# Kernel tuning notes

Measured on AMD Instinct MI355X. Metric: run time of the kernel, lower is better.

The kernel has to match this reference:

```python
import jax, jax.numpy as jnp
import numpy as np

B, H, W, C = 32, 56, 56, 256
NH, WS, SH = 8, 7, 3
HD = C // NH
SCALE = HD ** -0.5
N = WS * WS
MLP = 4 * C


def _rel_pos_index():
    coords = np.stack(np.meshgrid(np.arange(WS), np.arange(WS), indexing='ij')).reshape(2, -1)
    rel = (coords[:, :, None] - coords[:, None, :]).transpose(1, 2, 0)
    rel[..., 0] += WS - 1
    rel[..., 1] += WS - 1
    rel[..., 0] *= 2 * WS - 1
    return jnp.asarray(rel.sum(-1))  # (N, N) int


def _attn_mask():
    # standard Swin shifted-window mask, computed statically
    img = np.zeros((H, W))
    cnt = 0
    for hs in (slice(0, -WS), slice(-WS, -SH), slice(-SH, None)):
        for ws_ in (slice(0, -WS), slice(-WS, -SH), slice(-SH, None)):
            img[hs, ws_] = cnt
            cnt += 1
    mw = img.reshape(H // WS, WS, W // WS, WS).transpose(0, 2, 1, 3).reshape(-1, N)
    am = mw[:, None, :] - mw[:, :, None]
    am = np.where(am != 0, -1e9, 0.0).astype(np.float32)
    return jnp.asarray(am)  # (nW, N, N)


def _part(x):
    b = x.shape[0]
    x = x.reshape(b, H // WS, WS, W // WS, WS, C)
    return x.transpose(0, 1, 3, 2, 4, 5).reshape(-1, N, C)


def _rev(xw):
    x = xw.reshape(-1, H // WS, W // WS, WS, WS, C)
    return x.transpose(0, 1, 3, 2, 4, 5).reshape(-1, H, W, C)


def _ln(x, g, b):
    m = x.mean(-1, keepdims=True)
    v = x.var(-1, keepdims=True)
    return (x - m) / jnp.sqrt(v + 1e-5) * g + b


def setup_inputs() -> dict:
    key = jax.random.key(0)
    ks = jax.random.split(key, 6)
    s = 0.02
    return {
        'x': jax.random.normal(ks[0], (B, H, W, C), jnp.float32),
        'gamma1': jnp.ones((C,), jnp.float32),
        'beta1': jnp.zeros((C,), jnp.float32),
        'w_qkv': jax.random.normal(ks[1], (C, 3 * C), jnp.float32) * s,
        'b_qkv': jnp.zeros((3 * C,), jnp.float32),
        'rpb': jax.random.normal(ks[2], ((2 * WS - 1) ** 2, NH), jnp.float32) * s,
        'w_proj': jax.random.normal(ks[3], (C, C), jnp.float32) * s,
        'b_proj': jnp.zeros((C,), jnp.float32),
        'gamma2': jnp.ones((C,), jnp.float32),
        'beta2': jnp.zeros((C,), jnp.float32),
        'w_fc1': jax.random.normal(ks[4], (C, MLP), jnp.float32) * s,
        'b_fc1': jnp.zeros((MLP,), jnp.float32),
        'w_fc2': jax.random.normal(ks[5], (MLP, C), jnp.float32) * s,
        'b_fc2': jnp.zeros((C,), jnp.float32),
    }


def reference(x, gamma1, beta1, w_qkv, b_qkv, rpb, w_proj, b_proj, gamma2, beta2, w_fc1, b_fc1, w_fc2, b_fc2):
    idx = _rel_pos_index()
    mask = _attn_mask()  # (nW, N, N)
    nW = mask.shape[0]

    shortcut = x
    xn = _ln(x, gamma1, beta1)
    xs = jnp.roll(xn, (-SH, -SH), axis=(1, 2))        # cyclic shift
    xw = _part(xs)                                     # (B*nW, N, C)

    qkv = (xw @ w_qkv + b_qkv).reshape(-1, N, 3, NH, HD).transpose(2, 0, 3, 1, 4)
    # SNN-variant IF (ReLU) gates on q, k, v
    q, k, v = jax.nn.relu(qkv[0]), jax.nn.relu(qkv[1]), jax.nn.relu(qkv[2])

    attn = jnp.einsum('bhnd,bhmd->bhnm', q * SCALE, k)  # (B*nW, NH, N, N)
    bias = rpb[idx].transpose(2, 0, 1)                  # (NH, N, N)
    attn = attn + bias[None]
    attn = attn.reshape(-1, nW, NH, N, N) + mask[None, :, None]
    attn = attn.reshape(-1, NH, N, N)
    # stdp_qk ReLU before softmax (faithful to source)
    attn = jax.nn.softmax(jax.nn.relu(attn), axis=-1)
    # stdp_av ReLU on attention output
    out = jax.nn.relu(jnp.einsum('bhnm,bhmd->bhnd', attn, v))
    out = out.transpose(0, 2, 1, 3).reshape(-1, N, C) @ w_proj + b_proj

    xs = _rev(out)
    x = shortcut + jnp.roll(xs, (SH, SH), axis=(1, 2))  # reverse shift + residual

    h = jax.nn.gelu(_ln(x, gamma2, beta2) @ w_fc1 + b_fc1, approximate=False)
    return x + h @ w_fc2 + b_fc2
```

## Files before the change

kernel.cpp:

```cpp
#include <hip/hip_runtime.h>
#include <stdint.h>

typedef unsigned short u16;
typedef short bf16x8 __attribute__((ext_vector_type(8)));
typedef float f32x4 __attribute__((ext_vector_type(4)));

#define NTOK 100352
#define NWIN 2048
#define CC 256
#define NHEAD 8
#define HDIM 32
#define NWT 49
#define MLPD 1024
#define ATT_SCALE 0.17677669529663687f

__device__ __forceinline__ u16 f2b(float f) {
  union { float f; uint32_t u; } c; c.f = f;
  return (u16)((c.u + 0x7fffu + ((c.u >> 16) & 1u)) >> 16);
}
__device__ __forceinline__ float b2f(u16 h) {
  union { uint32_t u; float f; } c; c.u = ((uint32_t)h) << 16;
  return c.f;
}
__device__ __forceinline__ uint32_t f2b2(float lo, float hi) {
  uint32_t r;
  asm("v_cvt_pk_bf16_f32 %0, %1, %2" : "=v"(r) : "v"(lo), "v"(hi));
  return r;
}

__device__ __forceinline__ void gload_lds16(const void* g, void* l) {
  __builtin_amdgcn_global_load_lds((const __attribute__((address_space(1))) void*)g,
                                   (__attribute__((address_space(3))) void*)l, 16, 0, 0);
}

__global__ __launch_bounds__(256)
void prep_k(const float* __restrict__ wqkv, const float* __restrict__ wproj,
            const float* __restrict__ wfc1, const float* __restrict__ wfc2,
            const float* __restrict__ rpb,
            u16* __restrict__ qkvT, u16* __restrict__ projT,
            u16* __restrict__ fc1T, u16* __restrict__ fc2T, float* __restrict__ lut) {
  int i = blockIdx.x * 256 + threadIdx.x;
  if (i < 196608) {
    int k = i / 768, n = i % 768;
    qkvT[(size_t)n * 256 + k] = f2b(wqkv[i]);
  } else if (i < 262144) {
    int j = i - 196608, k = j / 256, n = j % 256;
    projT[(size_t)n * 256 + k] = f2b(wproj[j]);
  } else if (i < 524288) {
    int j = i - 262144, k = j / 1024, n = j % 1024;
    fc1T[(size_t)n * 256 + k] = f2b(wfc1[j]);
  } else if (i < 786432) {
    int j = i - 524288, k = j / 256, n = j % 256;
    fc2T[(size_t)n * 1024 + k] = f2b(wfc2[j]);
  } else if (i < 819200) {
    int j = i - 786432;
    int h = j >> 12, m = (j >> 6) & 63, n = j & 63;
    float v = 0.f;
    if (m < 49 && n < 49) {
      int i1 = n / 7, j1 = n % 7, i2 = m / 7, j2 = m % 7;
      v = rpb[((i1 - i2 + 6) * 13 + (j1 - j2 + 6)) * 8 + h];
    }
    lut[j] = v;
  }
}

__global__ __launch_bounds__(256)
void ln_k(const float* __restrict__ x, const float* __restrict__ g,
          const float* __restrict__ be, u16* __restrict__ out) {
  int token = blockIdx.x * 4 + (threadIdx.x >> 6);
  int lane = threadIdx.x & 63;
  int win = token / 49, nn = token % 49;
  int b = win >> 6, wh = (win >> 3) & 7, ww = win & 7;
  int i = nn / 7, j = nn % 7;
  int h = wh * 7 + i + 3; if (h >= 56) h -= 56;
  int w = ww * 7 + j + 3; if (w >= 56) w -= 56;
  size_t src = ((size_t)((b * 56 + h) * 56 + w)) * CC;
  f32x4 v = *(const f32x4*)&x[src + lane * 4];
  float s1 = v[0] + v[1] + v[2] + v[3];
  float s2 = v[0]*v[0] + v[1]*v[1] + v[2]*v[2] + v[3]*v[3];
#pragma unroll
  for (int o = 32; o; o >>= 1) { s1 += __shfl_xor(s1, o); s2 += __shfl_xor(s2, o); }
  float mean = s1 * (1.f / 256.f);
  float var = s2 * (1.f / 256.f) - mean * mean;
  float rstd = rsqrtf(var + 1e-5f);
  f32x4 gv = *(const f32x4*)&g[lane * 4];
  f32x4 bv = *(const f32x4*)&be[lane * 4];
  float y0 = (v[0]-mean)*rstd*gv[0] + bv[0];
  float y1 = (v[1]-mean)*rstd*gv[1] + bv[1];
  float y2 = (v[2]-mean)*rstd*gv[2] + bv[2];
  float y3 = (v[3]-mean)*rstd*gv[3] + bv[3];
  *(uint2*)&out[(size_t)token * CC + lane * 4] = make_uint2(f2b2(y0, y1), f2b2(y2, y3));
}

#define BM 128
#define BN 128
enum { EPI_QKV = 0, EPI_GELU = 2, EPI_FC2 = 3 };

template<int EPI, int NKT>
__global__ __launch_bounds__(256)
void gemm_k(const u16* __restrict__ A, const u16* __restrict__ BT,
            const float* __restrict__ bias,
            void* __restrict__ p0, const void* __restrict__ p1) {
  constexpr int K = NKT * 64;
  __shared__ u16 aL[2][BM * 64];
  __shared__ u16 bL[BN * 64];
  const int tid = threadIdx.x;
  const int lane = tid & 63;
  const int wv = tid >> 6;
  const int wm = wv >> 1, wn = wv & 1;

  int bx = blockIdx.x, by = blockIdx.y;
  {
    int nwg = gridDim.x * gridDim.y;
    int lin = by * gridDim.x + bx;
    int q = nwg >> 3, r = nwg & 7;
    int xcd = lin & 7, idx = lin >> 3;
    int wg = (xcd < r ? xcd * (q + 1) : r * (q + 1) + (xcd - r) * q) + idx;
    bx = wg % gridDim.x;
    by = wg / gridDim.x;
  }
  const long m0 = (long)by * BM;
  const int n0 = bx * BN;

  f32x4 acc[4][4] = {};
  const int r15 = lane & 15;
  const int g4 = lane >> 4;

  const u16* pA[4];
  const u16* pB[4];
  int lslot[4];
#pragma unroll
  for (int it = 0; it < 4; ++it) {
    int slot = tid + 256 * it;
    int row = slot >> 3, c8 = slot & 7;
    int cs = c8 ^ (row & 7);
    pA[it] = &A[(m0 + row) * K + cs * 8];
    pB[it] = &BT[(size_t)(n0 + row) * K + cs * 8];
    lslot[it] = slot * 8;
  }
  int aoff[2][4], boff[2][4];
#pragma unroll
  for (int kk = 0; kk < 2; ++kk)
#pragma unroll
    for (int m = 0; m < 4; ++m) {
      int rowa = wm * 64 + m * 16 + r15;
      aoff[kk][m] = rowa * 64 + (((kk * 4 + g4) ^ (rowa & 7)) << 3);
      int rowb = wn * 64 + m * 16 + r15;
      boff[kk][m] = rowb * 64 + (((kk * 4 + g4) ^ (rowb & 7)) << 3);
    }

  auto stageA = [&](int bufi) {
#pragma unroll
    for (int it = 0; it < 4; ++it) { gload_lds16(pA[it], &aL[bufi][lslot[it]]); pA[it] += 64; }
  };
  auto stageB = [&]() {
#pragma unroll
    for (int it = 0; it < 4; ++it) { gload_lds16(pB[it], &bL[lslot[it]]); pB[it] += 64; }
  };

  stageB();
  stageA(0);
  stageA(1);

  for (int t = 0; t < NKT; ++t) {
    if (t + 1 < NKT) asm volatile("s_waitcnt vmcnt(4)" ::: "memory");
    else             asm volatile("s_waitcnt vmcnt(0)" ::: "memory");
    __builtin_amdgcn_sched_barrier(0);
    __builtin_amdgcn_s_barrier();
    __builtin_amdgcn_sched_barrier(0);
    {
      const u16* ab = aL[t & 1];
#pragma unroll
      for (int kk = 0; kk < 2; ++kk) {
        bf16x8 af[4], bfr[4];
#pragma unroll
        for (int m = 0; m < 4; ++m) af[m] = *(const bf16x8*)&ab[aoff[kk][m]];
#pragma unroll
        for (int n = 0; n < 4; ++n) bfr[n] = *(const bf16x8*)&bL[boff[kk][n]];
#pragma unroll
        for (int n = 0; n < 4; ++n)
#pragma unroll
          for (int m = 0; m < 4; ++m)
            acc[n][m] = __builtin_amdgcn_mfma_f32_16x16x32_bf16(bfr[n], af[m], acc[n][m], 0, 0, 0);
      }
    }
    __builtin_amdgcn_sched_barrier(0);
    __builtin_amdgcn_s_barrier();
    __builtin_amdgcn_sched_barrier(0);
    if (t + 1 < NKT) stageB();
    if (t + 2 < NKT) stageA(t & 1);
  }

#pragma unroll
  for (int mt = 0; mt < 4; ++mt) {
    const int mrow = (int)m0 + wm * 64 + mt * 16 + r15;
    int win = 0, nn = 0;
    if (EPI == EPI_QKV) { win = mrow / 49; nn = mrow - win * 49; }
#pragma unroll
    for (int nt = 0; nt < 4; ++nt) {
      const int col0 = n0 + wn * 64 + nt * 16 + g4 * 4;
      f32x4 bv = *(const f32x4*)&bias[col0];
      f32x4 v;
#pragma unroll
      for (int j = 0; j < 4; ++j) v[j] = acc[nt][mt][j] + bv[j];
      if (EPI == EPI_QKV) {
        int s = col0 >> 8, head = (col0 >> 5) & 7, d0 = col0 & 31;
        float sc = (s == 0) ? ATT_SCALE : 1.f;
#pragma unroll
        for (int j = 0; j < 4; ++j) v[j] = fmaxf(v[j], 0.f) * sc;
        u16* dst = (u16*)p0 + (size_t)s * ((size_t)NTOK * CC);
        *(uint2*)&dst[(((size_t)(win * NHEAD + head)) * NWT + nn) * HDIM + d0] =
            make_uint2(f2b2(v[0], v[1]), f2b2(v[2], v[3]));
      } else if (EPI == EPI_GELU) {
#pragma unroll
        for (int j = 0; j < 4; ++j) {
          float u = 0.79788456f * (v[j] + 0.044715f * v[j] * v[j] * v[j]);
          float th = 1.f - 2.f / (__expf(2.f * u) + 1.f);
          v[j] = 0.5f * v[j] * (1.f + th);
        }
        *(uint2*)&((u16*)p0)[(size_t)mrow * MLPD + col0] =
            make_uint2(f2b2(v[0], v[1]), f2b2(v[2], v[3]));
      } else {
        size_t idx = (size_t)mrow * CC + col0;
        f32x4 r = *(const f32x4*)&((const float*)p1)[idx];
#pragma unroll
        for (int j = 0; j < 4; ++j) v[j] += r[j];
        *(f32x4*)&((float*)p0)[idx] = v;
      }
    }
  }
}

__global__ __launch_bounds__(512)
void gemm_ln_k(const u16* __restrict__ A, const u16* __restrict__ BT,
               const float* __restrict__ bias, const float* __restrict__ xres,
               const float* __restrict__ g2, const float* __restrict__ be2,
               float* __restrict__ x2, u16* __restrict__ xn2) {
  constexpr int K = 256;
  constexpr int NKT = 4;
  __shared__ u16 aL[2][128 * 64];
  __shared__ u16 bL[256 * 64];
  __shared__ float st[4 * 128 * 2];
  const int tid = threadIdx.x;
  const int lane = tid & 63;
  const int wv = tid >> 6;
  const int wm = wv >> 2;
  const int wn = wv & 3;
  const int r15 = lane & 15;
  const int g4 = lane >> 4;

  int by = blockIdx.x;
  {
    int nwg = gridDim.x;
    int q = nwg >> 3, r = nwg & 7;
    int xcd = by & 7, idx = by >> 3;
    by = (xcd < r ? xcd * (q + 1) : r * (q + 1) + (xcd - r) * q) + idx;
  }
  const long m0 = (long)by * 128;

  f32x4 acc[4][4] = {};

  const u16* pA[2];
  int la[2];
#pragma unroll
  for (int it = 0; it < 2; ++it) {
    int slot = tid + 512 * it;
    int row = slot >> 3, c8 = slot & 7;
    int cs = c8 ^ (row & 7);
    pA[it] = &A[(m0 + row) * K + cs * 8];
    la[it] = slot * 8;
  }
  const u16* pB[4];
  int lb[4];
#pragma unroll
  for (int it = 0; it < 4; ++it) {
    int slot = tid + 512 * it;
    int row = slot >> 3, c8 = slot & 7;
    int cs = c8 ^ (row & 7);
    pB[it] = &BT[(size_t)row * K + cs * 8];
    lb[it] = slot * 8;
  }
  int aoff[2][4], boff[2][4];
#pragma unroll
  for (int kk = 0; kk < 2; ++kk)
#pragma unroll
    for (int m = 0; m < 4; ++m) {
      int rowa = wm * 64 + m * 16 + r15;
      aoff[kk][m] = rowa * 64 + (((kk * 4 + g4) ^ (rowa & 7)) << 3);
      int rowb = wn * 64 + m * 16 + r15;
      boff[kk][m] = rowb * 64 + (((kk * 4 + g4) ^ (rowb & 7)) << 3);
    }

  auto stageA = [&](int bufi) {
#pragma unroll
    for (int it = 0; it < 2; ++it) { gload_lds16(pA[it], &aL[bufi][la[it]]); pA[it] += 64; }
  };
  auto stageB = [&]() {
#pragma unroll
    for (int it = 0; it < 4; ++it) { gload_lds16(pB[it], &bL[lb[it]]); pB[it] += 64; }
  };

  stageB();
  stageA(0);
  stageA(1);

  for (int t = 0; t < NKT; ++t) {
    if (t + 1 < NKT) asm volatile("s_waitcnt vmcnt(2)" ::: "memory");
    else             asm volatile("s_waitcnt vmcnt(0)" ::: "memory");
    __builtin_amdgcn_sched_barrier(0);
    __builtin_amdgcn_s_barrier();
    __builtin_amdgcn_sched_barrier(0);
    {
      const u16* ab = aL[t & 1];
#pragma unroll
      for (int kk = 0; kk < 2; ++kk) {
        bf16x8 af[4], bfr[4];
#pragma unroll
        for (int m = 0; m < 4; ++m) af[m] = *(const bf16x8*)&ab[aoff[kk][m]];
#pragma unroll
        for (int n = 0; n < 4; ++n) bfr[n] = *(const bf16x8*)&bL[boff[kk][n]];
#pragma unroll
        for (int n = 0; n < 4; ++n)
#pragma unroll
          for (int m = 0; m < 4; ++m)
            acc[n][m] = __builtin_amdgcn_mfma_f32_16x16x32_bf16(bfr[n], af[m], acc[n][m], 0, 0, 0);
      }
    }
    __builtin_amdgcn_sched_barrier(0);
    __builtin_amdgcn_s_barrier();
    __builtin_amdgcn_sched_barrier(0);
    if (t + 1 < NKT) stageB();
    if (t + 2 < NKT) stageA(t & 1);
  }

  size_t pix[4];
  float s1[4] = {}, s2[4] = {};
#pragma unroll
  for (int mt = 0; mt < 4; ++mt) {
    const int mrow = (int)m0 + wm * 64 + mt * 16 + r15;
    int win = mrow / 49, nn = mrow - win * 49;
    int b = win >> 6, wh = (win >> 3) & 7, ww = win & 7;
    int i = nn / 7, jj = nn - i * 7;
    int h = wh * 7 + i + 3; if (h >= 56) h -= 56;
    int w = ww * 7 + jj + 3; if (w >= 56) w -= 56;
    pix[mt] = (size_t)((b * 56 + h) * 56 + w);
#pragma unroll
    for (int nt = 0; nt < 4; ++nt) {
      const int col0 = wn * 64 + nt * 16 + g4 * 4;
      f32x4 bv = *(const f32x4*)&bias[col0];
      f32x4 r = *(const f32x4*)&xres[pix[mt] * CC + col0];
      f32x4 v;
#pragma unroll
      for (int j = 0; j < 4; ++j) {
        v[j] = acc[nt][mt][j] + bv[j] + r[j];
        s1[mt] += v[j];
        s2[mt] += v[j] * v[j];
      }
      *(f32x4*)&x2[pix[mt] * CC + col0] = v;
      acc[nt][mt] = v;
    }
    s1[mt] += __shfl_xor(s1[mt], 16);  s1[mt] += __shfl_xor(s1[mt], 32);
    s2[mt] += __shfl_xor(s2[mt], 16);  s2[mt] += __shfl_xor(s2[mt], 32);
    if (g4 == 0) {
      int wrow = wm * 64 + mt * 16 + r15;
      st[(wn * 128 + wrow) * 2 + 0] = s1[mt];
      st[(wn * 128 + wrow) * 2 + 1] = s2[mt];
    }
  }
  __syncthreads();
#pragma unroll
  for (int mt = 0; mt < 4; ++mt) {
    int wrow = wm * 64 + mt * 16 + r15;
    float t1 = 0.f, t2 = 0.f;
#pragma unroll
    for (int w2 = 0; w2 < 4; ++w2) {
      t1 += st[(w2 * 128 + wrow) * 2 + 0];
      t2 += st[(w2 * 128 + wrow) * 2 + 1];
    }
    float mean = t1 * (1.f / 256.f);
    float var = t2 * (1.f / 256.f) - mean * mean;
    float rstd = rsqrtf(var + 1e-5f);
#pragma unroll
    for (int nt = 0; nt < 4; ++nt) {
      const int col0 = wn * 64 + nt * 16 + g4 * 4;
      f32x4 gv = *(const f32x4*)&g2[col0];
      f32x4 bv = *(const f32x4*)&be2[col0];
      float y0 = (acc[nt][mt][0] - mean) * rstd * gv[0] + bv[0];
      float y1 = (acc[nt][mt][1] - mean) * rstd * gv[1] + bv[1];
      float y2 = (acc[nt][mt][2] - mean) * rstd * gv[2] + bv[2];
      float y3 = (acc[nt][mt][3] - mean) * rstd * gv[3] + bv[3];
      *(uint2*)&xn2[pix[mt] * CC + col0] = make_uint2(f2b2(y0, y1), f2b2(y2, y3));
    }
  }
}

__global__ __launch_bounds__(256)
void attn_mfma_k(const u16* __restrict__ q, const u16* __restrict__ k2,
                 const u16* __restrict__ v2, const float* __restrict__ lut,
                 u16* __restrict__ out) {
  __shared__ u16 P_lds[4][64 * 72];
  const int tid = threadIdx.x;
  const int wv = tid >> 6;
  const int lane = tid & 63;
  const int c = lane & 15;
  const int g = lane >> 4;
  const int blk = blockIdx.x * 4 + wv;
  const int head = blk & 7;
  const int win = blk >> 3;
  const int wimg = win & 63;
  const int wh = wimg >> 3, ww = wimg & 7;
  const size_t base = (size_t)blk * (NWT * HDIM);
  u16* Pw = P_lds[wv];

  bf16x8 kf[4], qf[4];
#pragma unroll
  for (int t = 0; t < 4; ++t) {
    kf[t] = *(const bf16x8*)&k2[base + (size_t)(t * 16 + c) * HDIM + g * 8];
    qf[t] = *(const bf16x8*)&q [base + (size_t)(t * 16 + c) * HDIM + g * 8];
  }
  bf16x8 vf[2][2];
#pragma unroll
  for (int kcc = 0; kcc < 2; ++kcc)
#pragma unroll
    for (int td = 0; td < 2; ++td)
#pragma unroll
      for (int jj = 0; jj < 8; ++jj) {
        int m = kcc * 32 + g * 8 + jj;
        m = m < 49 ? m : 48;
        vf[kcc][td][jj] = (short)v2[base + (size_t)m * HDIM + td * 16 + c];
      }

  f32x4 acc[4][4] = {};
#pragma unroll
  for (int tm = 0; tm < 4; ++tm)
#pragma unroll
    for (int tn = 0; tn < 4; ++tn)
      acc[tm][tn] = __builtin_amdgcn_mfma_f32_16x16x32_bf16(kf[tm], qf[tn], acc[tm][tn], 0, 0, 0);

  const float* lrow = &lut[(size_t)head * 64 * 64];
  int Ln[4];
#pragma unroll
  for (int tn = 0; tn < 4; ++tn) {
    int n = tn * 16 + c;
    int i1 = (n * 9363) >> 16;
    int j1 = n - i1 * 7;
    int rh = (wh < 7) ? 0 : (i1 < 4 ? 1 : 2);
    int rw = (ww < 7) ? 0 : (j1 < 4 ? 1 : 2);
    Ln[tn] = rh * 3 + rw;
  }
  float colmax[4] = {0.f, 0.f, 0.f, 0.f};
#pragma unroll
  for (int tm = 0; tm < 4; ++tm)
#pragma unroll
    for (int j = 0; j < 4; ++j) {
      int m = tm * 16 + g * 4 + j;
      int i2 = (m * 9363) >> 16;
      int j2 = m - i2 * 7;
      int rh = (wh < 7) ? 0 : (i2 < 4 ? 1 : 2);
      int rw = (ww < 7) ? 0 : (j2 < 4 ? 1 : 2);
      int Lm = rh * 3 + rw;
#pragma unroll
      for (int tn = 0; tn < 4; ++tn) {
        float s = acc[tm][tn][j] + lrow[m * 64 + tn * 16 + c];
        s = fmaxf(s, 0.f);
        if (Lm != Ln[tn]) s = 0.f;
        acc[tm][tn][j] = s;
        colmax[tn] = fmaxf(colmax[tn], s);
      }
    }
#pragma unroll
  for (int tn = 0; tn < 4; ++tn) {
    colmax[tn] = fmaxf(colmax[tn], __shfl_xor(colmax[tn], 16));
    colmax[tn] = fmaxf(colmax[tn], __shfl_xor(colmax[tn], 32));
  }
  float colsum[4] = {0.f, 0.f, 0.f, 0.f};
#pragma unroll
  for (int tm = 0; tm < 4; ++tm)
#pragma unroll
    for (int j = 0; j < 4; ++j) {
      int m = tm * 16 + g * 4 + j;
      bool mvalid = (m < NWT);
#pragma unroll
      for (int tn = 0; tn < 4; ++tn) {
        float e = mvalid ? __expf(acc[tm][tn][j] - colmax[tn]) : 0.f;
        acc[tm][tn][j] = e;
        colsum[tn] += e;
      }
    }
#pragma unroll
  for (int tn = 0; tn < 4; ++tn) {
    colsum[tn] += __shfl_xor(colsum[tn], 16);
    colsum[tn] += __shfl_xor(colsum[tn], 32);
    colsum[tn] = 1.f / colsum[tn];
  }

#pragma unroll
  for (int tn = 0; tn < 4; ++tn) {
    int n = tn * 16 + c;
#pragma unroll
    for (int tm = 0; tm < 4; ++tm) {
      float r = colsum[tn];
      *(uint2*)&Pw[n * 72 + tm * 16 + g * 4] =
          make_uint2(f2b2(acc[tm][tn][0] * r, acc[tm][tn][1] * r),
                     f2b2(acc[tm][tn][2] * r, acc[tm][tn][3] * r));
    }
  }

  f32x4 oacc[4][2] = {};
#pragma unroll
  for (int kcc = 0; kcc < 2; ++kcc) {
    bf16x8 pf[4];
#pragma unroll
    for (int tr = 0; tr < 4; ++tr)
      pf[tr] = *(const bf16x8*)&Pw[(tr * 16 + c) * 72 + kcc * 32 + g * 8];
#pragma unroll
    for (int tr = 0; tr < 4; ++tr)
#pragma unroll
      for (int td = 0; td < 2; ++td)
        oacc[tr][td] = __builtin_amdgcn_mfma_f32_16x16x32_bf16(pf[tr], vf[kcc][td], oacc[tr][td], 0, 0, 0);
  }

#pragma unroll
  for (int tr = 0; tr < 4; ++tr)
#pragma unroll
    for (int j = 0; j < 4; ++j) {
      int n = tr * 16 + g * 4 + j;
      if (n < NWT) {
#pragma unroll
        for (int td = 0; td < 2; ++td) {
          int d = td * 16 + c;
          out[((size_t)(win * NWT + n)) * CC + head * HDIM + d] =
              f2b(fmaxf(oacc[tr][td][j], 0.f));
        }
      }
    }
}

extern "C" void kernel_launch(void* const* d_in, const int* in_sizes, int n_in,
                              void* d_out, int out_size, void* d_ws, size_t ws_size,
                              hipStream_t stream) {
  const float* x      = (const float*)d_in[0];
  const float* gamma1 = (const float*)d_in[1];
  const float* beta1  = (const float*)d_in[2];
  const float* w_qkv  = (const float*)d_in[3];
  const float* b_qkv  = (const float*)d_in[4];
  const float* rpb    = (const float*)d_in[5];
  const float* w_proj = (const float*)d_in[6];
  const float* b_proj = (const float*)d_in[7];
  const float* gamma2 = (const float*)d_in[8];
  const float* beta2  = (const float*)d_in[9];
  const float* w_fc1  = (const float*)d_in[10];
  const float* b_fc1  = (const float*)d_in[11];
  const float* w_fc2  = (const float*)d_in[12];
  const float* b_fc2  = (const float*)d_in[13];
  float* out = (float*)d_out;

  char* ws = (char*)d_ws;
  size_t off = 0;
  auto alloc = [&](size_t bytes) { void* p = ws + off; off = (off + bytes + 255) & ~(size_t)255; return p; };

  u16* wqkvT = (u16*)alloc(768 * 256 * 2);
  u16* wprojT = (u16*)alloc(256 * 256 * 2);
  u16* wfc1T = (u16*)alloc(1024 * 256 * 2);
  u16* wfc2T = (u16*)alloc(256 * 1024 * 2);
  float* lut = (float*)alloc(8 * 64 * 64 * 4);
  u16* region2 = (u16*)alloc((size_t)NTOK * CC * 2);
  char* region1 = (char*)alloc((size_t)3 * NTOK * CC * 2);

  u16* xw = region2;
  u16* qb = (u16*)region1;
  u16* kb = qb + (size_t)NTOK * CC;
  u16* vb = kb + (size_t)NTOK * CC;
  u16* attn_out = region2;
  float* x2 = (float*)region1;
  u16* xn2 = (u16*)(region1 + (size_t)NTOK * CC * 4);
  u16* hbuf = region2;

  if (ws_size < off) return;

  prep_k<<<3200, 256, 0, stream>>>(w_qkv, w_proj, w_fc1, w_fc2, rpb,
                                   wqkvT, wprojT, wfc1T, wfc2T, lut);

  ln_k<<<NTOK / 4, 256, 0, stream>>>(x, gamma1, beta1, xw);

  gemm_k<EPI_QKV, 4><<<dim3(768 / BN, NTOK / BM), 256, 0, stream>>>(
      xw, wqkvT, b_qkv, (void*)qb, nullptr);

  attn_mfma_k<<<NWIN * NHEAD / 4, 256, 0, stream>>>(qb, kb, vb, lut, attn_out);

  gemm_ln_k<<<NTOK / 128, 512, 0, stream>>>(
      attn_out, wprojT, b_proj, x, gamma2, beta2, x2, xn2);

  const int MCH = 25088;
  for (int c = 0; c < 4; ++c) {
    const u16* a1 = xn2 + (size_t)c * MCH * CC;
    gemm_k<EPI_GELU, 4><<<dim3(MLPD / BN, MCH / BM), 256, 0, stream>>>(
        a1, wfc1T, b_fc1, (void*)hbuf, nullptr);
    gemm_k<EPI_FC2, 16><<<dim3(CC / BN, MCH / BM), 256, 0, stream>>>(
        hbuf, wfc2T, b_fc2, (void*)(out + (size_t)c * MCH * CC),
        (const void*)(x2 + (size_t)c * MCH * CC));
  }
}
```

Measured before the change: 523.4 us.

## Keep post-attention residual in bf16 window order and scatter in FC2 epilogue

The proj+LN kernel now writes the intermediate residual x2 as bf16 instead of fp32, and writes both x2 and the normalized xn2 in window-token order rather than scattering them to pixel order. The FC2 epilogue reads the bf16 residual contiguously and performs the window-reverse and shift scatter when writing the final fp32 output. This halves residual traffic, makes the intermediate writes contiguous, and moves the scatter to the last store. The cost is bf16 rounding of the residual stream, which loses precision in the final output.

```diff
diff --git a/kernel.cpp b/kernel.cpp
--- a/kernel.cpp
+++ b/kernel.cpp
@@ -100,7 +100,7 @@
 __global__ __launch_bounds__(256)
 void gemm_k(const u16* __restrict__ A, const u16* __restrict__ BT,
             const float* __restrict__ bias,
-            void* __restrict__ p0, const void* __restrict__ p1) {
+            void* __restrict__ p0, const void* __restrict__ p1, int row0) {
   constexpr int K = NKT * 64;
   __shared__ u16 aL[2][BM * 64];
   __shared__ u16 bL[BN * 64];
@@ -195,7 +195,17 @@
   for (int mt = 0; mt < 4; ++mt) {
     const int mrow = (int)m0 + wm * 64 + mt * 16 + r15;
     int win = 0, nn = 0;
+    size_t pix = 0;
     if (EPI == EPI_QKV) { win = mrow / 49; nn = mrow - win * 49; }
+    if (EPI == EPI_FC2) {
+      int token = row0 + mrow;
+      win = token / 49; nn = token - win * 49;
+      int b = win >> 6, wh = (win >> 3) & 7, ww = win & 7;
+      int i = nn / 7, jj = nn - i * 7;
+      int h = wh * 7 + i + 3; if (h >= 56) h -= 56;
+      int w = ww * 7 + jj + 3; if (w >= 56) w -= 56;
+      pix = (size_t)((b * 56 + h) * 56 + w);
+    }
 #pragma unroll
     for (int nt = 0; nt < 4; ++nt) {
       const int col0 = n0 + wn * 64 + nt * 16 + g4 * 4;
@@ -221,11 +231,12 @@
         *(uint2*)&((u16*)p0)[(size_t)mrow * MLPD + col0] =
             make_uint2(f2b2(v[0], v[1]), f2b2(v[2], v[3]));
       } else {
-        size_t idx = (size_t)mrow * CC + col0;
-        f32x4 r = *(const f32x4*)&((const float*)p1)[idx];
-#pragma unroll
-        for (int j = 0; j < 4; ++j) v[j] += r[j];
-        *(f32x4*)&((float*)p0)[idx] = v;
+        uint2 rb = *(const uint2*)&((const u16*)p1)[(size_t)(row0 + mrow) * CC + col0];
+        v[0] += b2f((u16)(rb.x & 0xffffu));
+        v[1] += b2f((u16)(rb.x >> 16));
+        v[2] += b2f((u16)(rb.y & 0xffffu));
+        v[3] += b2f((u16)(rb.y >> 16));
+        *(f32x4*)&((float*)p0)[pix * CC + col0] = v;
       }
     }
   }
@@ -235,7 +246,7 @@
 void gemm_ln_k(const u16* __restrict__ A, const u16* __restrict__ BT,
                const float* __restrict__ bias, const float* __restrict__ xres,
                const float* __restrict__ g2, const float* __restrict__ be2,
-               float* __restrict__ x2, u16* __restrict__ xn2) {
+               u16* __restrict__ x2, u16* __restrict__ xn2) {
   constexpr int K = 256;
   constexpr int NKT = 4;
   __shared__ u16 aL[2][128 * 64];
@@ -356,7 +367,8 @@
         s1[mt] += v[j];
         s2[mt] += v[j] * v[j];
       }
-      *(f32x4*)&x2[pix[mt] * CC + col0] = v;
+      *(uint2*)&x2[(size_t)mrow * CC + col0] =
+          make_uint2(f2b2(v[0], v[1]), f2b2(v[2], v[3]));
       acc[nt][mt] = v;
     }
     s1[mt] += __shfl_xor(s1[mt], 16);  s1[mt] += __shfl_xor(s1[mt], 32);
@@ -370,6 +382,7 @@
   __syncthreads();
 #pragma unroll
   for (int mt = 0; mt < 4; ++mt) {
+    const int mrow = (int)m0 + wm * 64 + mt * 16 + r15;
     int wrow = wm * 64 + mt * 16 + r15;
     float t1 = 0.f, t2 = 0.f;
 #pragma unroll
@@ -389,7 +402,7 @@
       float y1 = (acc[nt][mt][1] - mean) * rstd * gv[1] + bv[1];
       float y2 = (acc[nt][mt][2] - mean) * rstd * gv[2] + bv[2];
       float y3 = (acc[nt][mt][3] - mean) * rstd * gv[3] + bv[3];
-      *(uint2*)&xn2[pix[mt] * CC + col0] = make_uint2(f2b2(y0, y1), f2b2(y2, y3));
+      *(uint2*)&xn2[(size_t)mrow * CC + col0] = make_uint2(f2b2(y0, y1), f2b2(y2, y3));
     }
   }
 }
@@ -572,8 +585,8 @@
   u16* kb = qb + (size_t)NTOK * CC;
   u16* vb = kb + (size_t)NTOK * CC;
   u16* attn_out = region2;
-  float* x2 = (float*)region1;
-  u16* xn2 = (u16*)(region1 + (size_t)NTOK * CC * 4);
+  u16* x2 = (u16*)region1;
+  u16* xn2 = x2 + (size_t)NTOK * CC;
   u16* hbuf = region2;
 
   if (ws_size < off) return;
@@ -584,7 +597,7 @@
   ln_k<<<NTOK / 4, 256, 0, stream>>>(x, gamma1, beta1, xw);
 
   gemm_k<EPI_QKV, 4><<<dim3(768 / BN, NTOK / BM), 256, 0, stream>>>(
-      xw, wqkvT, b_qkv, (void*)qb, nullptr);
+      xw, wqkvT, b_qkv, (void*)qb, nullptr, 0);
 
   attn_mfma_k<<<NWIN * NHEAD / 4, 256, 0, stream>>>(qb, kb, vb, lut, attn_out);
 
@@ -595,9 +608,8 @@
   for (int c = 0; c < 4; ++c) {
     const u16* a1 = xn2 + (size_t)c * MCH * CC;
     gemm_k<EPI_GELU, 4><<<dim3(MLPD / BN, MCH / BM), 256, 0, stream>>>(
-        a1, wfc1T, b_fc1, (void*)hbuf, nullptr);
+        a1, wfc1T, b_fc1, (void*)hbuf, nullptr, 0);
     gemm_k<EPI_FC2, 16><<<dim3(CC / BN, MCH / BM), 256, 0, stream>>>(
-        hbuf, wfc2T, b_fc2, (void*)(out + (size_t)c * MCH * CC),
-        (const void*)(x2 + (size_t)c * MCH * CC));
-  }
-}
+        hbuf, wfc2T, b_fc2, (void*)out, (const void*)x2, c * MCH);
+  }
+}
```

Result: no change. 516.3 us (-1.4%).
